# Kernel tuning notes

Hardware: AMD Instinct MI355X
Metric: run time of the kernel (lower is better)

Reference implementation:

```python
import jax, jax.numpy as jnp
import numpy as np

D_MODEL = 2048
N_HEADS = 16
N_KV_HEADS = 2
HEAD_DIM = D_MODEL // N_HEADS  # 128
N_REP = N_HEADS // N_KV_HEADS  # 8
SCALE = HEAD_DIM ** -0.5


def setup_inputs() -> dict:
    key = jax.random.key(0)
    ks = jax.random.split(key, 5)
    B, N = 2, 2048
    x = jax.random.normal(ks[0], (B, N, D_MODEL), dtype=jnp.float32)
    # weights stored as [in, out] (math identical to torch Linear x @ W.T)
    s = D_MODEL ** -0.5
    Wq = jax.random.normal(ks[1], (D_MODEL, D_MODEL), dtype=jnp.float32) * s
    Wk = jax.random.normal(ks[2], (D_MODEL, N_KV_HEADS * HEAD_DIM), dtype=jnp.float32) * s
    Wv = jax.random.normal(ks[3], (D_MODEL, N_KV_HEADS * HEAD_DIM), dtype=jnp.float32) * s
    Wo = jax.random.normal(ks[4], (D_MODEL, D_MODEL), dtype=jnp.float32) * s
    return {"x": x, "Wq": Wq, "Wk": Wk, "Wv": Wv, "Wo": Wo}


def reference(x, Wq, Wk, Wv, Wo):
    B, N, C = x.shape
    q = (x @ Wq).reshape(B, N, N_HEADS, HEAD_DIM).transpose(0, 2, 1, 3)      # [B,H,N,hd]
    k = (x @ Wk).reshape(B, N, N_KV_HEADS, HEAD_DIM).transpose(0, 2, 1, 3)   # [B,Hkv,N,hd]
    v = (x @ Wv).reshape(B, N, N_KV_HEADS, HEAD_DIM).transpose(0, 2, 1, 3)
    if N_REP > 1:
        k = jnp.repeat(k, N_REP, axis=1)  # [B,H,N,hd]
        v = jnp.repeat(v, N_REP, axis=1)
    attn = jnp.einsum('bhnd,bhmd->bhnm', q, k) * SCALE
    attn = jax.nn.softmax(attn, axis=-1)
    out = jnp.einsum('bhnm,bhmd->bhnd', attn, v)
    out = out.transpose(0, 2, 1, 3).reshape(B, N, C)
    return out @ Wo
```

## Files before the change

kernel.cpp:

```cpp
#include <hip/hip_runtime.h>

typedef unsigned short u16;
typedef __attribute__((ext_vector_type(4))) float floatx4;
typedef __attribute__((ext_vector_type(8))) __bf16 bf16x8;
typedef __attribute__((ext_vector_type(8))) u16 u16x8;

#define D_MODEL 2048
#define SEQ     2048
#define NH      16
#define NKV     2
#define HD      128
#define QKVN    2560
#define SCALE   0.08838834764831845f
#define QSCALE  (0.08838834764831845f * 1.4426950408889634f)
#define M_STATIC 20.0f

__device__ __forceinline__ u16 f2bf(float f) {
    unsigned int x = __float_as_uint(f);
    return (u16)((x + 0x7fffu + ((x >> 16) & 1u)) >> 16);
}
__device__ __forceinline__ u16 cvt_scale(float f, float s) { return f2bf(f * s); }
__device__ __forceinline__ u16 cvt_scale(u16 f, float)     { return f; }

__device__ __forceinline__ void gload16(const u16* g, u16* l) {
    __builtin_amdgcn_global_load_lds((const __attribute__((address_space(1))) void*)g,
                                     (__attribute__((address_space(3))) void*)l, 16, 0, 0);
}

__global__ void f2b_k(const float* __restrict__ src, u16* __restrict__ dst, long n)
{
    long i = ((long)blockIdx.x * blockDim.x + threadIdx.x) * 8;
    if (i >= n) return;
    float4 a = *(const float4*)(src + i);
    float4 b = *(const float4*)(src + i + 4);
    u16x8 o;
    o[0] = f2bf(a.x); o[1] = f2bf(a.y); o[2] = f2bf(a.z); o[3] = f2bf(a.w);
    o[4] = f2bf(b.x); o[5] = f2bf(b.y); o[6] = f2bf(b.z); o[7] = f2bf(b.w);
    *(u16x8*)(dst + i) = o;
}

template <typename T>
__global__ void tr_k(const T* __restrict__ src, u16* __restrict__ dst,
                     int ld_s, int ld_d, long sbs, long dbs, float scale)
{
    __shared__ T tile[32][33];
    src += (long)blockIdx.z * sbs;
    dst += (long)blockIdx.z * dbs;
    int c0 = blockIdx.x * 32, r0 = blockIdx.y * 32;
    int tx = threadIdx.x, ty = threadIdx.y;
#pragma unroll
    for (int i = 0; i < 32; i += 8)
        tile[ty + i][tx] = src[(long)(r0 + ty + i) * ld_s + c0 + tx];
    __syncthreads();
#pragma unroll
    for (int i = 0; i < 32; i += 8)
        dst[(long)(c0 + ty + i) * ld_d + r0 + tx] = cvt_scale(tile[tx][ty + i], scale);
}

template <bool F32OUT>
__global__ __launch_bounds__(256, 2) void gemm_bt_k(
    const u16* __restrict__ A, const u16* __restrict__ Bt, void* __restrict__ Cv,
    int K, int lda, int ldb, int ldc)
{
    __shared__ __align__(16) u16 As[128 * 64];
    __shared__ __align__(16) u16 Bs[128 * 64];
    const int tid  = threadIdx.x;
    const int wave = tid >> 6, lane = tid & 63;
    const int quad = lane >> 4, l16 = lane & 15;
    const long bm = (long)blockIdx.x * 128;
    const long bn = (long)blockIdx.y * 128;
    const int wr = (wave >> 1) * 64;
    const int wc = (wave & 1) * 64;

    floatx4 acc[4][4] = {};

    for (long k0 = 0; k0 < K; k0 += 64) {
#pragma unroll
        for (int t = 0; t < 4; ++t) {
            int c = tid + t * 256;
            int row = c >> 3, sl = c & 7;
            int kc = sl ^ (row & 7);
            gload16(A + (bm + row) * lda + k0 + kc * 8,
                    As + ((tid & ~63) + t * 256) * 8);
        }
#pragma unroll
        for (int t = 0; t < 4; ++t) {
            int c = tid + t * 256;
            int row = c >> 3, sl = c & 7;
            int kc = sl ^ (row & 7);
            gload16(Bt + (bn + row) * ldb + k0 + kc * 8,
                    Bs + ((tid & ~63) + t * 256) * 8);
        }
        __syncthreads();

#pragma unroll
        for (int ks = 0; ks < 2; ++ks) {
            bf16x8 af[4], bfr[4];
#pragma unroll
            for (int mt = 0; mt < 4; ++mt) {
                int r  = wr + mt * 16 + l16;
                int ch = (ks * 4 + quad) ^ (r & 7);
                af[mt] = *(const bf16x8*)(As + r * 64 + ch * 8);
            }
#pragma unroll
            for (int nt = 0; nt < 4; ++nt) {
                int r  = wc + nt * 16 + l16;
                int ch = (ks * 4 + quad) ^ (r & 7);
                bfr[nt] = *(const bf16x8*)(Bs + r * 64 + ch * 8);
            }
#pragma unroll
            for (int mt = 0; mt < 4; ++mt)
#pragma unroll
                for (int nt = 0; nt < 4; ++nt)
                    acc[mt][nt] = __builtin_amdgcn_mfma_f32_16x16x32_bf16(
                        af[mt], bfr[nt], acc[mt][nt], 0, 0, 0);
        }
        __syncthreads();
    }

#pragma unroll
    for (int mt = 0; mt < 4; ++mt)
#pragma unroll
        for (int nt = 0; nt < 4; ++nt)
#pragma unroll
            for (int r = 0; r < 4; ++r) {
                long row = bm + wr + mt * 16 + quad * 4 + r;
                long col = bn + wc + nt * 16 + l16;
                if (F32OUT) ((float*)Cv)[row * ldc + col] = acc[mt][nt][r];
                else        ((u16*)Cv)[row * ldc + col]   = f2bf(acc[mt][nt][r]);
            }
}

#define KTILE (64 * 128)
#define VTILE (128 * 64)

__global__ __launch_bounds__(512, 4) void attn_k(
    const u16* __restrict__ QKV, const u16* __restrict__ Vt, u16* __restrict__ Out)
{
    __shared__ __align__(16) u16 smem[2 * KTILE + 2 * VTILE + 128 * 64];

    const int tid  = threadIdx.x;
    const int wave = tid >> 6, lane = tid & 63;
    const int quad = lane >> 4, l16 = lane & 15;
    const int qs = wave & 3;
    const int kh = wave >> 2;
    const int qt = blockIdx.x, h = blockIdx.y, b = blockIdx.z;
    const int kvh = h >> 3;

    const long qrow0 = (long)b * SEQ + (long)qt * 128;
    const u16* Qbase = QKV + qrow0 * QKVN + h * HD;
    const u16* Kbase = QKV + (long)b * SEQ * QKVN + D_MODEL + kvh * HD;
    const u16* Vbase = Vt + ((long)b * NKV + kvh) * (long)HD * SEQ;
    u16* const P = smem + 2 * KTILE + 2 * VTILE;

#pragma unroll
    for (int t = 0; t < 4; ++t) {
        int c = tid + t * 512;
        int row = c >> 4, sl = c & 15;
        int dc = sl ^ (row & 15);
        gload16(Qbase + (long)row * QKVN + dc * 8, smem + ((tid & ~63) + t * 512) * 8);
    }
    __syncthreads();

    bf16x8 qa[2][4];
#pragma unroll
    for (int mt = 0; mt < 2; ++mt)
#pragma unroll
        for (int ks = 0; ks < 4; ++ks) {
            int r  = qs * 32 + mt * 16 + l16;
            int ch = (ks * 4 + quad) ^ (r & 15);
            qa[mt][ks] = *(const bf16x8*)(smem + r * 128 + ch * 8);
        }
    __syncthreads();

    floatx4 o[2][4] = {};
    float l_run[2] = { 0.f, 0.f };

    {
        u16* Kn = smem;
        u16* Vn = smem + 2 * KTILE;
#pragma unroll
        for (int t = 0; t < 2; ++t) {
            int c = tid + t * 512;
            int row = c >> 4, sl = c & 15;
            int dc = sl ^ (row & 15);
            gload16(Kbase + (long)row * QKVN + dc * 8, Kn + ((tid & ~63) + t * 512) * 8);
        }
#pragma unroll
        for (int t = 0; t < 2; ++t) {
            int c = tid + t * 512;
            int row = c >> 3, sl = c & 7;
            int kc = sl ^ (row & 7);
            gload16(Vbase + (long)row * SEQ + kc * 8, Vn + ((tid & ~63) + t * 512) * 8);
        }
    }
    __syncthreads();

    for (int t = 0; t < SEQ / 64; ++t) {
        const int cur = t & 1;
        const u16* Kc = smem + cur * KTILE;
        const u16* Vc = smem + 2 * KTILE + cur * VTILE;

        if (t + 1 < SEQ / 64) {
            u16* Kn = smem + (cur ^ 1) * KTILE;
            u16* Vn = smem + 2 * KTILE + (cur ^ 1) * VTILE;
            const long k0n = (long)(t + 1) * 64;
#pragma unroll
            for (int tt = 0; tt < 2; ++tt) {
                int c = tid + tt * 512;
                int row = c >> 4, sl = c & 15;
                int dc = sl ^ (row & 15);
                gload16(Kbase + (k0n + row) * QKVN + dc * 8,
                        Kn + ((tid & ~63) + tt * 512) * 8);
            }
#pragma unroll
            for (int tt = 0; tt < 2; ++tt) {
                int c = tid + tt * 512;
                int row = c >> 3, sl = c & 7;
                int kc = sl ^ (row & 7);
                gload16(Vbase + (long)row * SEQ + k0n + kc * 8,
                        Vn + ((tid & ~63) + tt * 512) * 8);
            }
        }

        floatx4 s[2][2] = {};
        __builtin_amdgcn_s_setprio(1);
#pragma unroll
        for (int ks = 0; ks < 4; ++ks) {
            bf16x8 kb[2];
#pragma unroll
            for (int nt = 0; nt < 2; ++nt) {
                int r  = kh * 32 + nt * 16 + l16;
                int ch = (ks * 4 + quad) ^ (r & 15);
                kb[nt] = *(const bf16x8*)(Kc + r * 128 + ch * 8);
            }
#pragma unroll
            for (int mt = 0; mt < 2; ++mt)
#pragma unroll
                for (int nt = 0; nt < 2; ++nt)
                    s[mt][nt] = __builtin_amdgcn_mfma_f32_16x16x32_bf16(
                        kb[nt], qa[mt][ks], s[mt][nt], 0, 0, 0);
        }
        __builtin_amdgcn_s_setprio(0);

#pragma unroll
        for (int mt = 0; mt < 2; ++mt) {
#pragma unroll
            for (int nt = 0; nt < 2; ++nt)
#pragma unroll
                for (int r = 0; r < 4; ++r)
                    s[mt][nt][r] = __builtin_amdgcn_exp2f(s[mt][nt][r] - M_STATIC);
            float ta = (s[mt][0][0] + s[mt][0][1]) + (s[mt][0][2] + s[mt][0][3]);
            float tb = (s[mt][1][0] + s[mt][1][1]) + (s[mt][1][2] + s[mt][1][3]);
            float sum = ta + tb;
            sum += __shfl_xor(sum, 16);
            sum += __shfl_xor(sum, 32);
            l_run[mt] += sum;

            int row = qs * 32 + mt * 16 + l16;
            int swz = row & 7;
            u16* base = P + row * 64 + (quad & 1) * 4;
#pragma unroll
            for (int nt = 0; nt < 2; ++nt) {
                unsigned int lo, hi;
                asm("v_cvt_pk_bf16_f32 %0, %1, %2"
                    : "=v"(lo) : "v"(s[mt][nt][0]), "v"(s[mt][nt][1]));
                asm("v_cvt_pk_bf16_f32 %0, %1, %2"
                    : "=v"(hi) : "v"(s[mt][nt][2]), "v"(s[mt][nt][3]));
                int chunk = (kh * 4 + nt * 2 + (quad >> 1)) ^ swz;
                uint2 val; val.x = lo; val.y = hi;
                *(uint2*)(base + chunk * 8) = val;
            }
        }

        asm volatile("s_waitcnt lgkmcnt(0)" ::: "memory");
        __builtin_amdgcn_sched_barrier(0);
        __builtin_amdgcn_s_barrier();

        __builtin_amdgcn_s_setprio(1);
#pragma unroll
        for (int ks = 0; ks < 2; ++ks) {
            bf16x8 pa[2];
#pragma unroll
            for (int mt = 0; mt < 2; ++mt) {
                int row = qs * 32 + mt * 16 + l16;
                int chk = (ks * 4 + quad) ^ (row & 7);
                pa[mt] = *(const bf16x8*)(P + row * 64 + chk * 8);
            }
#pragma unroll
            for (int dt = 0; dt < 4; ++dt) {
                int r  = kh * 64 + dt * 16 + l16;
                int ch = (ks * 4 + quad) ^ (r & 7);
                bf16x8 vb = *(const bf16x8*)(Vc + r * 64 + ch * 8);
#pragma unroll
                for (int mt = 0; mt < 2; ++mt)
                    o[mt][dt] = __builtin_amdgcn_mfma_f32_16x16x32_bf16(
                        pa[mt], vb, o[mt][dt], 0, 0, 0);
            }
        }
        __builtin_amdgcn_s_setprio(0);
        __syncthreads();
    }

    float* lbuf = (float*)P;
    if (quad == 0) {
        lbuf[(qs * 2 + kh) * 32 + l16]      = l_run[0];
        lbuf[(qs * 2 + kh) * 32 + 16 + l16] = l_run[1];
    }
    __syncthreads();
#pragma unroll
    for (int mt = 0; mt < 2; ++mt)
#pragma unroll
        for (int r = 0; r < 4; ++r) {
            int qq = mt * 16 + quad * 4 + r;
            float lt = lbuf[(qs * 2) * 32 + qq] + lbuf[(qs * 2 + 1) * 32 + qq];
            float inv = 1.f / lt;
            long row = qrow0 + qs * 32 + qq;
#pragma unroll
            for (int dt = 0; dt < 4; ++dt)
                Out[row * D_MODEL + h * HD + kh * 64 + dt * 16 + l16] =
                    f2bf(o[mt][dt][r] * inv);
        }
}

extern "C" void kernel_launch(void* const* d_in, const int* in_sizes, int n_in,
                              void* d_out, int out_size, void* d_ws, size_t ws_size,
                              hipStream_t stream)
{
    const float* X  = (const float*)d_in[0];
    const float* Wq = (const float*)d_in[1];
    const float* Wk = (const float*)d_in[2];
    const float* Wv = (const float*)d_in[3];
    const float* Wo = (const float*)d_in[4];
    float* out = (float*)d_out;

    u16* Xb    = (u16*)d_ws;
    u16* attn  = Xb;
    u16* WtQKV = Xb + (long)4096 * D_MODEL;
    u16* WtO   = WtQKV + (long)QKVN * D_MODEL;
    u16* QKV   = WtO + (long)D_MODEL * D_MODEL;
    u16* Vt    = QKV + (long)4096 * QKVN;

    f2b_k<<<dim3(4096), 256, 0, stream>>>(X, Xb, (long)4096 * D_MODEL);

    dim3 tb(32, 8);
    tr_k<float><<<dim3(64, 64, 1), tb, 0, stream>>>(Wq, WtQKV, 2048, 2048, 0, 0, QSCALE);
    tr_k<float><<<dim3(8, 64, 1), tb, 0, stream>>>(Wk, WtQKV + 2048L * 2048, 256, 2048, 0, 0, 1.f);
    tr_k<float><<<dim3(8, 64, 1), tb, 0, stream>>>(Wv, WtQKV + 2304L * 2048, 256, 2048, 0, 0, 1.f);
    tr_k<float><<<dim3(64, 64, 1), tb, 0, stream>>>(Wo, WtO, 2048, 2048, 0, 0, 1.f);

    gemm_bt_k<false><<<dim3(32, 20), 256, 0, stream>>>(Xb, WtQKV, QKV, 2048, 2048, 2048, QKVN);

    tr_k<u16><<<dim3(8, 64, 2), tb, 0, stream>>>(QKV + 2304, Vt, QKVN, 2048,
                                                 (long)SEQ * QKVN, 256L * 2048, 1.f);

    attn_k<<<dim3(16, NH, 2), 512, 0, stream>>>(QKV, Vt, attn);

    gemm_bt_k<true><<<dim3(32, 16), 256, 0, stream>>>(attn, WtO, out, 2048, 2048, 2048, 2048);
}
```

Before: 280.7 us.

## Load K fragments directly from global into registers and change LDS swizzle

Removes the double-buffered K tile from LDS. Each wave now loads its K MFMA fragments straight from global memory into registers, prefetching the next tile after the QK^T MFMAs. This cuts LDS usage, which may allow higher occupancy, and drops the LDS write/read traffic for K. It also changes the XOR swizzle for V and P to (row&7)^((row>>1)&4) to reduce bank conflicts. The cost is uncoalesced 16-byte global loads per lane with latency exposed inside the loop, and K is re-read from global or L2 by both kh wave groups instead of being shared through LDS.

```diff
diff --git a/kernel.cpp b/kernel.cpp
--- a/kernel.cpp
+++ b/kernel.cpp
@@ -131,13 +131,13 @@
             }
 }
 
-#define KTILE (64 * 128)
 #define VTILE (128 * 64)
+#define NT    (SEQ / 64)
 
 __global__ __launch_bounds__(512, 4) void attn_k(
     const u16* __restrict__ QKV, const u16* __restrict__ Vt, u16* __restrict__ Out)
 {
-    __shared__ __align__(16) u16 smem[2 * KTILE + 2 * VTILE + 128 * 64];
+    __shared__ __align__(16) u16 smem[2 * VTILE + 128 * 64];
 
     const int tid  = threadIdx.x;
     const int wave = tid >> 6, lane = tid & 63;
@@ -151,7 +151,7 @@
     const u16* Qbase = QKV + qrow0 * QKVN + h * HD;
     const u16* Kbase = QKV + (long)b * SEQ * QKVN + D_MODEL + kvh * HD;
     const u16* Vbase = Vt + ((long)b * NKV + kvh) * (long)HD * SEQ;
-    u16* const P = smem + 2 * KTILE + 2 * VTILE;
+    u16* const P = smem + 2 * VTILE;
 
 #pragma unroll
     for (int t = 0; t < 4; ++t) {
@@ -173,51 +173,40 @@
         }
     __syncthreads();
 
+    const long KADV = 64L * QKVN;
+    const u16* kp0 = Kbase + (long)(kh * 32 + l16) * QKVN + quad * 8;
+    const u16* kp1 = kp0 + 16L * QKVN;
+    bf16x8 kb[2][4];
+#pragma unroll
+    for (int ks = 0; ks < 4; ++ks) {
+        kb[0][ks] = *(const bf16x8*)(kp0 + ks * 32);
+        kb[1][ks] = *(const bf16x8*)(kp1 + ks * 32);
+    }
+
     floatx4 o[2][4] = {};
     float l_run[2] = { 0.f, 0.f };
 
-    {
-        u16* Kn = smem;
-        u16* Vn = smem + 2 * KTILE;
-#pragma unroll
-        for (int t = 0; t < 2; ++t) {
-            int c = tid + t * 512;
-            int row = c >> 4, sl = c & 15;
-            int dc = sl ^ (row & 15);
-            gload16(Kbase + (long)row * QKVN + dc * 8, Kn + ((tid & ~63) + t * 512) * 8);
-        }
-#pragma unroll
-        for (int t = 0; t < 2; ++t) {
-            int c = tid + t * 512;
-            int row = c >> 3, sl = c & 7;
-            int kc = sl ^ (row & 7);
-            gload16(Vbase + (long)row * SEQ + kc * 8, Vn + ((tid & ~63) + t * 512) * 8);
-        }
-    }
-    __syncthreads();
-
-    for (int t = 0; t < SEQ / 64; ++t) {
+#pragma unroll
+    for (int t = 0; t < 2; ++t) {
+        int c = tid + t * 512;
+        int row = c >> 3, sl = c & 7;
+        int kc = sl ^ ((row & 7) ^ ((row >> 1) & 4));
+        gload16(Vbase + (long)row * SEQ + kc * 8, smem + ((tid & ~63) + t * 512) * 8);
+    }
+    __syncthreads();
+
+    for (int t = 0; t < NT; ++t) {
         const int cur = t & 1;
-        const u16* Kc = smem + cur * KTILE;
-        const u16* Vc = smem + 2 * KTILE + cur * VTILE;
-
-        if (t + 1 < SEQ / 64) {
-            u16* Kn = smem + (cur ^ 1) * KTILE;
-            u16* Vn = smem + 2 * KTILE + (cur ^ 1) * VTILE;
+        const u16* Vc = smem + cur * VTILE;
+
+        if (t + 1 < NT) {
+            u16* Vn = smem + (cur ^ 1) * VTILE;
             const long k0n = (long)(t + 1) * 64;
-#pragma unroll
-            for (int tt = 0; tt < 2; ++tt) {
-                int c = tid + tt * 512;
-                int row = c >> 4, sl = c & 15;
-                int dc = sl ^ (row & 15);
-                gload16(Kbase + (k0n + row) * QKVN + dc * 8,
-                        Kn + ((tid & ~63) + tt * 512) * 8);
-            }
 #pragma unroll
             for (int tt = 0; tt < 2; ++tt) {
                 int c = tid + tt * 512;
                 int row = c >> 3, sl = c & 7;
-                int kc = sl ^ (row & 7);
+                int kc = sl ^ ((row & 7) ^ ((row >> 1) & 4));
                 gload16(Vbase + (long)row * SEQ + k0n + kc * 8,
                         Vn + ((tid & ~63) + tt * 512) * 8);
             }
@@ -226,22 +215,23 @@
         floatx4 s[2][2] = {};
         __builtin_amdgcn_s_setprio(1);
 #pragma unroll
-        for (int ks = 0; ks < 4; ++ks) {
-            bf16x8 kb[2];
-#pragma unroll
-            for (int nt = 0; nt < 2; ++nt) {
-                int r  = kh * 32 + nt * 16 + l16;
-                int ch = (ks * 4 + quad) ^ (r & 15);
-                kb[nt] = *(const bf16x8*)(Kc + r * 128 + ch * 8);
-            }
+        for (int ks = 0; ks < 4; ++ks)
 #pragma unroll
             for (int mt = 0; mt < 2; ++mt)
 #pragma unroll
                 for (int nt = 0; nt < 2; ++nt)
                     s[mt][nt] = __builtin_amdgcn_mfma_f32_16x16x32_bf16(
-                        kb[nt], qa[mt][ks], s[mt][nt], 0, 0, 0);
-        }
+                        kb[nt][ks], qa[mt][ks], s[mt][nt], 0, 0, 0);
         __builtin_amdgcn_s_setprio(0);
+
+        if (t + 1 < NT) {
+            const long adv = (long)(t + 1) * KADV;
+#pragma unroll
+            for (int ks = 0; ks < 4; ++ks) {
+                kb[0][ks] = *(const bf16x8*)(kp0 + adv + ks * 32);
+                kb[1][ks] = *(const bf16x8*)(kp1 + adv + ks * 32);
+            }
+        }
 
 #pragma unroll
         for (int mt = 0; mt < 2; ++mt) {
@@ -258,7 +248,7 @@
             l_run[mt] += sum;
 
             int row = qs * 32 + mt * 16 + l16;
-            int swz = row & 7;
+            int m = (row & 7) ^ ((row >> 1) & 4);
             u16* base = P + row * 64 + (quad & 1) * 4;
 #pragma unroll
             for (int nt = 0; nt < 2; ++nt) {
@@ -267,7 +257,7 @@
                     : "=v"(lo) : "v"(s[mt][nt][0]), "v"(s[mt][nt][1]));
                 asm("v_cvt_pk_bf16_f32 %0, %1, %2"
                     : "=v"(hi) : "v"(s[mt][nt][2]), "v"(s[mt][nt][3]));
-                int chunk = (kh * 4 + nt * 2 + (quad >> 1)) ^ swz;
+                int chunk = (kh * 4 + nt * 2 + (quad >> 1)) ^ m;
                 uint2 val; val.x = lo; val.y = hi;
                 *(uint2*)(base + chunk * 8) = val;
             }
@@ -284,13 +274,15 @@
 #pragma unroll
             for (int mt = 0; mt < 2; ++mt) {
                 int row = qs * 32 + mt * 16 + l16;
-                int chk = (ks * 4 + quad) ^ (row & 7);
+                int m = (row & 7) ^ ((row >> 1) & 4);
+                int chk = (ks * 4 + quad) ^ m;
                 pa[mt] = *(const bf16x8*)(P + row * 64 + chk * 8);
             }
 #pragma unroll
             for (int dt = 0; dt < 4; ++dt) {
                 int r  = kh * 64 + dt * 16 + l16;
-                int ch = (ks * 4 + quad) ^ (r & 7);
+                int mv = (r & 7) ^ ((r >> 1) & 4);
+                int ch = (ks * 4 + quad) ^ mv;
                 bf16x8 vb = *(const bf16x8*)(Vc + r * 64 + ch * 8);
 #pragma unroll
                 for (int mt = 0; mt < 2; ++mt)
```

New measurement: 387.8 us. 1.38x slower.
